# Performance work log

Hardware: AMD Instinct MI355X
Metric: run time of the kernel (lower is better)

The kernel has to match this reference:

```python
import jax, jax.numpy as jnp
import numpy as np

D = 512
B = 64
T = 512

def setup_inputs() -> dict:
    key = jax.random.key(0)
    ks = jax.random.split(key, 9)
    s = 1.0 / np.sqrt(D)
    def w(k):
        return jax.random.uniform(k, (D, D), jnp.float32, -s, s)
    def b(k):
        return jax.random.uniform(k, (D,), jnp.float32, -s, s)
    return {
        "evidence_seq": jax.random.normal(ks[0], (B, T, D), jnp.float32),
        "We": w(ks[1]), "be": b(ks[2]),
        "Wp": w(ks[3]), "bp": b(ks[4]),
        "Wl": w(ks[5]), "bl": b(ks[6]),
        "Ww": w(ks[7]), "bw": b(ks[8]),
    }

def reference(evidence_seq, We, be, Wp, bp, Wl, bl, Ww, bw):
    # Precompute all input-side projections in batched GEMMs: (B,T,D)
    ev_proj = jnp.einsum('btd,de->bte', evidence_seq, We) + be
    leak = jax.nn.sigmoid(jnp.einsum('btd,de->bte', evidence_seq, Wl) + bl)
    write = jax.nn.sigmoid(jnp.einsum('btd,de->bte', evidence_seq, Ww) + bw)

    def step(belief_prev, inputs):
        ev_t, leak_t, write_t = inputs  # each (B, D)
        candidate = jnp.tanh(belief_prev @ Wp + bp + ev_t)
        belief = leak_t * belief_prev + write_t * candidate
        return belief, belief

    belief0 = jnp.zeros((evidence_seq.shape[0], We.shape[1]), evidence_seq.dtype)
    # scan over time axis: move T to leading dim
    xs = (jnp.swapaxes(ev_proj, 0, 1), jnp.swapaxes(leak, 0, 1), jnp.swapaxes(write, 0, 1))
    _, belief_seq_t = jax.lax.scan(step, belief0, xs)
    return jnp.swapaxes(belief_seq_t, 0, 1)  # (B, T, D)
```

## Files before the change

### kernel.cpp

```cpp
#include <hip/hip_runtime.h>
#include <math.h>

#define DD 512
#define TT 512

typedef __attribute__((ext_vector_type(8))) short short8;
typedef __attribute__((ext_vector_type(4))) float float4v;

static __device__ inline unsigned short f2bf(float f) {
    unsigned int b = __builtin_bit_cast(unsigned int, f);
    b += 0x7FFFu + ((b >> 16) & 1u);
    return (unsigned short)(b >> 16);
}
static __device__ inline float bf2f(unsigned short u) {
    unsigned int b = ((unsigned int)u) << 16;
    return __builtin_bit_cast(float, b);
}

__global__ __launch_bounds__(512) void proj_kernel(
    const float* __restrict__ X,
    const float* __restrict__ We, const float* __restrict__ be,
    const float* __restrict__ Wl, const float* __restrict__ bl,
    const float* __restrict__ Ww, const float* __restrict__ bw,
    float* __restrict__ Pe, unsigned short* __restrict__ Pl,
    unsigned short* __restrict__ Pw)
{
    __shared__ __align__(16) unsigned short Asw[8][64][8];
    __shared__ __align__(16) unsigned short Bsw[32][64][8];

    const int tid  = threadIdx.x;
    const int lane = tid & 63;
    const int wv   = tid >> 6;
    const int mat  = blockIdx.y;
    const int m0   = blockIdx.x * 128;

    const float* W    = (mat == 0) ? We : (mat == 1 ? Wl : Ww);
    const float* bias = (mat == 0) ? be : (mat == 1 ? bl : bw);

    float4v acc[32];
#pragma unroll
    for (int i = 0; i < 32; i++) acc[i] = (float4v){0.f, 0.f, 0.f, 0.f};

    for (int kc = 0; kc < 16; kc++) {
        __syncthreads();
#pragma unroll
        for (int i = 0; i < 2; i++) {
            int f = tid + 512 * i;
            int m = f >> 3;
            int k = (f & 7) * 4;
            float4v xv = *reinterpret_cast<const float4v*>(
                &X[(m0 + m) * DD + kc * 32 + k]);
            int mt = m >> 4;
            int ln = (m & 15) | (((k >> 3) & 3) << 4);
            int j  = k & 7;
            Asw[mt][ln][j + 0] = f2bf(xv.x);
            Asw[mt][ln][j + 1] = f2bf(xv.y);
            Asw[mt][ln][j + 2] = f2bf(xv.z);
            Asw[mt][ln][j + 3] = f2bf(xv.w);
        }
#pragma unroll
        for (int i = 0; i < 8; i++) {
            int f = tid + 512 * i;
            int k = f >> 7;
            int n = (f & 127) * 4;
            float4v wv4 = *reinterpret_cast<const float4v*>(
                &W[(kc * 32 + k) * DD + n]);
            int q  = (k >> 3) & 3;
            int j  = k & 7;
            int nt = n >> 4;
            int lb = (n & 15) | (q << 4);
            Bsw[nt][lb + 0][j] = f2bf(wv4.x);
            Bsw[nt][lb + 1][j] = f2bf(wv4.y);
            Bsw[nt][lb + 2][j] = f2bf(wv4.z);
            Bsw[nt][lb + 3][j] = f2bf(wv4.w);
        }
        __syncthreads();
        short8 a = *reinterpret_cast<const short8*>(&Asw[wv][lane][0]);
#pragma unroll
        for (int nt = 0; nt < 32; nt++) {
            short8 b = *reinterpret_cast<const short8*>(&Bsw[nt][lane][0]);
            acc[nt] = __builtin_amdgcn_mfma_f32_16x16x32_bf16(a, b, acc[nt], 0, 0, 0);
        }
    }

    const int q  = lane >> 4;
    const int c0 = lane & 15;
#pragma unroll
    for (int nt = 0; nt < 32; nt++) {
        int   col = nt * 16 + c0;
        float bv  = bias[col];
#pragma unroll
        for (int r = 0; r < 4; r++) {
            int row = m0 + wv * 16 + q * 4 + r;
            float v = acc[nt][r] + bv;
            int idx = row * DD + col;
            if (mat == 0) {
                Pe[idx] = v;
            } else {
                float s = 1.0f / (1.0f + expf(-v));
                if (mat == 1) Pl[idx] = f2bf(s);
                else          Pw[idx] = f2bf(s);
            }
        }
    }
}

__global__ __launch_bounds__(512) void rec_kernel(
    const float* __restrict__ Wp, const float* __restrict__ bp,
    const float* __restrict__ Pe, const unsigned short* __restrict__ Pl,
    const unsigned short* __restrict__ Pw,
    float* __restrict__ dout, unsigned* ex)
{
    __shared__ __align__(16) unsigned short Bsw[8][16][64][8];
    __shared__ __align__(16) unsigned short Asw[16][520];

    const int tid  = threadIdx.x;
    const int lane = tid & 63;
    const int wv   = tid >> 6;
    const int team = blockIdx.x & 7;
    const int wsl  = blockIdx.x >> 3;
    const int m0   = team * 8;
    const int n0   = wsl * 128;

    for (int i = 0; i < 32; i++) {
        int f  = tid + 512 * i;
        int k  = f >> 5;
        int nl = (f & 31) * 4;
        float4v w4 = *reinterpret_cast<const float4v*>(&Wp[k * DD + n0 + nl]);
        int kk = k >> 5;
        int qq = (k >> 3) & 3;
        int j  = k & 7;
        int nt = nl >> 4;
        int lb = (nl & 15) | (qq << 4);
        Bsw[nt][kk][lb + 0][j] = f2bf(w4.x);
        Bsw[nt][kk][lb + 1][j] = f2bf(w4.y);
        Bsw[nt][kk][lb + 2][j] = f2bf(w4.z);
        Bsw[nt][kk][lb + 3][j] = f2bf(w4.w);
    }
    for (int i = tid; i < 16 * 520; i += 512) ((unsigned short*)Asw)[i] = 0;
    __syncthreads();

    const int  qf     = lane >> 4;
    const int  c0     = lane & 15;
    const bool active = (qf < 2);
    const int  nep    = n0 + wv * 16 + c0;
    const int  ts     = wv * 32 + qf * 16 + c0;
    const float bpv   = bp[nep];
    float pv[4] = {0.f, 0.f, 0.f, 0.f};

    int pp[3];
#pragma unroll
    for (int p3 = 0; p3 < 3; p3++) pp[p3] = p3 + (p3 >= wsl ? 1 : 0);

    for (int t = 0; t < TT; t++) {
        float pe[4], lk[4], wr[4];
        int   idx[4];
        if (active) {
#pragma unroll
            for (int r = 0; r < 4; r++) {
                int brow = m0 + qf * 4 + r;
                idx[r] = (brow * TT + t) * DD + nep;
                pe[r]  = Pe[idx[r]];
                lk[r]  = bf2f(Pl[idx[r]]);
                wr[r]  = bf2f(Pw[idx[r]]);
            }
        }

        if (t > 0 && active) {
            const unsigned tg = (unsigned)(t - 1);
            unsigned* exb = ex + (unsigned)(((t - 1) & 1) * 8 + team) * 4096;
            const unsigned* ap[3];
#pragma unroll
            for (int p3 = 0; p3 < 3; p3++)
                ap[p3] = exb + pp[p3] * 1024 + ts * 4;

            unsigned w[12];
            bool ok;
            do {
#pragma unroll
                for (int p3 = 0; p3 < 3; p3++)
#pragma unroll
                    for (int r = 0; r < 4; r++)
                        w[p3 * 4 + r] = __hip_atomic_load(
                            ap[p3] + r, __ATOMIC_RELAXED, __HIP_MEMORY_SCOPE_AGENT);
                ok = true;
#pragma unroll
                for (int i = 0; i < 12; i++) ok &= ((w[i] & 0xFFFFu) == tg);
            } while (!ok);

#pragma unroll
            for (int p3 = 0; p3 < 3; p3++) {
                int col = pp[p3] * 128 + wv * 16 + c0;
#pragma unroll
                for (int r = 0; r < 4; r++)
                    Asw[qf * 4 + r][col] = (unsigned short)(w[p3 * 4 + r] >> 16);
            }
        }
        __syncthreads();

        float4v acc0 = {0.f, 0.f, 0.f, 0.f}, acc1 = {0.f, 0.f, 0.f, 0.f};
#pragma unroll
        for (int kk = 0; kk < 16; kk++) {
            short8 a = *reinterpret_cast<const short8*>(&Asw[c0][kk * 32 + qf * 8]);
            short8 b = *reinterpret_cast<const short8*>(&Bsw[wv][kk][lane][0]);
            if (kk & 1) acc1 = __builtin_amdgcn_mfma_f32_16x16x32_bf16(a, b, acc1, 0, 0, 0);
            else        acc0 = __builtin_amdgcn_mfma_f32_16x16x32_bf16(a, b, acc0, 0, 0, 0);
        }

        float bel[4];
        if (active) {
#pragma unroll
            for (int r = 0; r < 4; r++) {
                float pre  = acc0[r] + acc1[r] + bpv + pe[r];
                float cand = tanhf(pre);
                bel[r] = lk[r] * pv[r] + wr[r] * cand;
                pv[r]  = bel[r];
            }
        }
        __syncthreads();

        if (active) {
#pragma unroll
            for (int r = 0; r < 4; r++) Asw[qf * 4 + r][nep] = f2bf(bel[r]);
            unsigned* sp = ex + (unsigned)((t & 1) * 8 + team) * 4096
                              + wsl * 1024 + ts * 4;
#pragma unroll
            for (int r = 0; r < 4; r++) {
                unsigned wd = ((unsigned)f2bf(bel[r]) << 16) | (unsigned)(t & 0xFFFF);
                __hip_atomic_store(sp + r, wd, __ATOMIC_RELAXED,
                                   __HIP_MEMORY_SCOPE_AGENT);
            }
#pragma unroll
            for (int r = 0; r < 4; r++) dout[idx[r]] = bel[r];
        }
    }
}

extern "C" void kernel_launch(void* const* d_in, const int* in_sizes, int n_in,
                              void* d_out, int out_size, void* d_ws, size_t ws_size,
                              hipStream_t stream) {
    (void)in_sizes; (void)n_in; (void)out_size; (void)ws_size;
    const float* X  = (const float*)d_in[0];
    const float* We = (const float*)d_in[1];
    const float* be = (const float*)d_in[2];
    const float* Wp = (const float*)d_in[3];
    const float* bp = (const float*)d_in[4];
    const float* Wl = (const float*)d_in[5];
    const float* bl = (const float*)d_in[6];
    const float* Ww = (const float*)d_in[7];
    const float* bw = (const float*)d_in[8];
    float* out = (float*)d_out;

    char* ws = (char*)d_ws;
    float*          Pe = (float*)ws;
    unsigned short* Pl = (unsigned short*)(ws + 67108864);
    unsigned short* Pw = (unsigned short*)(ws + 100663296);
    unsigned*       ex = (unsigned*)(ws + 134217728);

    proj_kernel<<<dim3(256, 3), 512, 0, stream>>>(X, We, be, Wl, bl, Ww, bw,
                                                  Pe, Pl, Pw);
    rec_kernel<<<dim3(32), 512, 0, stream>>>(Wp, bp, Pe, Pl, Pw, out, ex);
}
```

Baseline: 2.023 ms.

## Replace cross-block atomic exchange with independent per-batch-slice recurrence blocks

The recurrence was split across 32 blocks that swapped belief slices every step through global atomics and spin-waits. It now runs on 4 blocks, each owning 16 batch rows and the full 512-wide Wp, so the per-step exchange uses only shared memory and __syncthreads. Most of Wp is held in registers as bf16, the belief tile in LDS is XOR-swizzled, and tanh is computed with __expf. The projection kernel now folds bp into the Pe bias, stores Pe as bf16 instead of fp32, and writes all three projections in a per-timestep page layout so each step reads contiguous uint2 loads. The trade-off is much less parallelism (4 CUs) with 4x more MFMA work per block, plus reduced precision on Pe.

After: 3.600 ms. 1.78x slower.

```diff
diff --git a/kernel.cpp b/kernel.cpp
--- a/kernel.cpp
+++ b/kernel.cpp
@@ -12,18 +12,21 @@
     b += 0x7FFFu + ((b >> 16) & 1u);
     return (unsigned short)(b >> 16);
 }
-static __device__ inline float bf2f(unsigned short u) {
-    unsigned int b = ((unsigned int)u) << 16;
-    return __builtin_bit_cast(float, b);
+static __device__ inline float bfhi(unsigned u) {
+    return __builtin_bit_cast(float, u & 0xFFFF0000u);
+}
+static __device__ inline float bflo(unsigned u) {
+    return __builtin_bit_cast(float, u << 16);
 }
 
 __global__ __launch_bounds__(512) void proj_kernel(
     const float* __restrict__ X,
     const float* __restrict__ We, const float* __restrict__ be,
+    const float* __restrict__ bp,
     const float* __restrict__ Wl, const float* __restrict__ bl,
     const float* __restrict__ Ww, const float* __restrict__ bw,
-    float* __restrict__ Pe, unsigned short* __restrict__ Pl,
-    unsigned short* __restrict__ Pw)
+    unsigned short* __restrict__ PeB, unsigned short* __restrict__ Pl2,
+    unsigned short* __restrict__ Pw2)
 {
     __shared__ __align__(16) unsigned short Asw[8][64][8];
     __shared__ __align__(16) unsigned short Bsw[32][64][8];
@@ -34,8 +37,7 @@
     const int mat  = blockIdx.y;
     const int m0   = blockIdx.x * 128;
 
-    const float* W    = (mat == 0) ? We : (mat == 1 ? Wl : Ww);
-    const float* bias = (mat == 0) ? be : (mat == 1 ? bl : bw);
+    const float* W = (mat == 0) ? We : (mat == 1 ? Wl : Ww);
 
     float4v acc[32];
 #pragma unroll
@@ -83,156 +85,152 @@
         }
     }
 
-    const int q  = lane >> 4;
-    const int c0 = lane & 15;
-#pragma unroll
-    for (int nt = 0; nt < 32; nt++) {
-        int   col = nt * 16 + c0;
-        float bv  = bias[col];
+    const int q     = lane >> 4;
+    const int c0    = lane & 15;
+    const int tbase = m0 & 511;
+    const int rb    = m0 >> 9;
+    const int b     = rb >> 4;
+    const int qft   = (rb & 15) >> 2;
+    const int rt    = rb & 3;
+
+    unsigned short* P = (mat == 0) ? PeB : (mat == 1 ? Pl2 : Pw2);
+
+#pragma unroll
+    for (int wt = 0; wt < 8; wt++) {
+        const int tidt = wt * 64 + qft * 16 + c0;
+        float bs[4];
+#pragma unroll
+        for (int n2 = 0; n2 < 4; n2++) {
+            const int col = (wt * 4 + n2) * 16 + c0;
+            bs[n2] = (mat == 0) ? (be[col] + bp[col])
+                                : ((mat == 1) ? bl[col] : bw[col]);
+        }
 #pragma unroll
         for (int r = 0; r < 4; r++) {
-            int row = m0 + wv * 16 + q * 4 + r;
-            float v = acc[nt][r] + bv;
-            int idx = row * DD + col;
-            if (mat == 0) {
-                Pe[idx] = v;
-            } else {
-                float s = 1.0f / (1.0f + expf(-v));
-                if (mat == 1) Pl[idx] = f2bf(s);
-                else          Pw[idx] = f2bf(s);
+            const int t    = tbase + wv * 16 + q * 4 + r;
+            const int page = (((t << 2) + b) << 2) + rt;
+            float v[4];
+#pragma unroll
+            for (int n2 = 0; n2 < 4; n2++) {
+                float x = acc[wt * 4 + n2][r] + bs[n2];
+                v[n2] = (mat == 0) ? x : (1.0f / (1.0f + expf(-x)));
             }
+            uint2 u;
+            u.x = (unsigned)f2bf(v[0]) | ((unsigned)f2bf(v[1]) << 16);
+            u.y = (unsigned)f2bf(v[2]) | ((unsigned)f2bf(v[3]) << 16);
+            *reinterpret_cast<uint2*>(&P[(page << 11) + (tidt << 2)]) = u;
         }
     }
 }
 
 __global__ __launch_bounds__(512) void rec_kernel(
-    const float* __restrict__ Wp, const float* __restrict__ bp,
-    const float* __restrict__ Pe, const unsigned short* __restrict__ Pl,
-    const unsigned short* __restrict__ Pw,
-    float* __restrict__ dout, unsigned* ex)
+    const float* __restrict__ Wp,
+    const unsigned short* __restrict__ PeB,
+    const unsigned short* __restrict__ Pl2,
+    const unsigned short* __restrict__ Pw2,
+    float* __restrict__ dout)
 {
-    __shared__ __align__(16) unsigned short Bsw[8][16][64][8];
-    __shared__ __align__(16) unsigned short Asw[16][520];
+    __shared__ __align__(16) unsigned short BswL[8][16][64][8];
+    __shared__ __align__(16) char AswP[16384];
 
     const int tid  = threadIdx.x;
     const int lane = tid & 63;
     const int wv   = tid >> 6;
-    const int team = blockIdx.x & 7;
-    const int wsl  = blockIdx.x >> 3;
-    const int m0   = team * 8;
-    const int n0   = wsl * 128;
-
-    for (int i = 0; i < 32; i++) {
-        int f  = tid + 512 * i;
-        int k  = f >> 5;
-        int nl = (f & 31) * 4;
-        float4v w4 = *reinterpret_cast<const float4v*>(&Wp[k * DD + n0 + nl]);
-        int kk = k >> 5;
-        int qq = (k >> 3) & 3;
-        int j  = k & 7;
-        int nt = nl >> 4;
-        int lb = (nl & 15) | (qq << 4);
-        Bsw[nt][kk][lb + 0][j] = f2bf(w4.x);
-        Bsw[nt][kk][lb + 1][j] = f2bf(w4.y);
-        Bsw[nt][kk][lb + 2][j] = f2bf(w4.z);
-        Bsw[nt][kk][lb + 3][j] = f2bf(w4.w);
-    }
-    for (int i = tid; i < 16 * 520; i += 512) ((unsigned short*)Asw)[i] = 0;
+    const int qf   = lane >> 4;
+    const int c0   = lane & 15;
+    const int blk  = blockIdx.x;
+
+    short8 bf[3][16];
+
+#pragma unroll
+    for (int nt = 0; nt < 4; nt++) {
+        for (int it = 0; it < 32; it++) {
+            const int f  = it * 64 + lane;
+            const int k  = f >> 2;
+            const int c4 = f & 3;
+            const float4v w4 = *reinterpret_cast<const float4v*>(
+                &Wp[(k << 9) + wv * 64 + nt * 16 + c4 * 4]);
+            const int kk = k >> 5;
+            const int qq = (k >> 3) & 3;
+            const int j  = k & 7;
+            const int lb = (c4 * 4) | (qq << 4);
+            BswL[wv][kk][lb + 0][j] = f2bf(w4.x);
+            BswL[wv][kk][lb + 1][j] = f2bf(w4.y);
+            BswL[wv][kk][lb + 2][j] = f2bf(w4.z);
+            BswL[wv][kk][lb + 3][j] = f2bf(w4.w);
+        }
+        if (nt < 3) {
+#pragma unroll
+            for (int kk = 0; kk < 16; kk++)
+                bf[nt][kk] = *reinterpret_cast<const short8*>(&BswL[wv][kk][lane][0]);
+        }
+    }
+
+#pragma unroll
+    for (int i = 0; i < 8; i++)
+        reinterpret_cast<unsigned*>(AswP)[tid + (i << 9)] = 0;
     __syncthreads();
 
-    const int  qf     = lane >> 4;
-    const int  c0     = lane & 15;
-    const bool active = (qf < 2);
-    const int  nep    = n0 + wv * 16 + c0;
-    const int  ts     = wv * 32 + qf * 16 + c0;
-    const float bpv   = bp[nep];
-    float pv[4] = {0.f, 0.f, 0.f, 0.f};
-
-    int pp[3];
-#pragma unroll
-    for (int p3 = 0; p3 < 3; p3++) pp[p3] = p3 + (p3 >= wsl ? 1 : 0);
+    float pv[4][4];
+#pragma unroll
+    for (int nt = 0; nt < 4; nt++)
+#pragma unroll
+        for (int r = 0; r < 4; r++) pv[nt][r] = 0.0f;
+
+    const int colb = wv * 64 + c0;
+    const int aswz = (c0 & 7) << 4;
+    const int arp  = (c0 << 10) + (qf << 4);
+    const int bq   = (blk << 4) + (qf << 2);
 
     for (int t = 0; t < TT; t++) {
-        float pe[4], lk[4], wr[4];
-        int   idx[4];
-        if (active) {
+        float4v acc[4];
+#pragma unroll
+        for (int i = 0; i < 4; i++) acc[i] = (float4v){0.f, 0.f, 0.f, 0.f};
+#pragma unroll
+        for (int kk = 0; kk < 16; kk++) {
+            const short8 a = *reinterpret_cast<const short8*>(
+                AswP + ((arp + (kk << 6)) ^ aswz));
+            const short8 b3 = *reinterpret_cast<const short8*>(&BswL[wv][kk][lane][0]);
+            acc[0] = __builtin_amdgcn_mfma_f32_16x16x32_bf16(a, bf[0][kk], acc[0], 0, 0, 0);
+            acc[1] = __builtin_amdgcn_mfma_f32_16x16x32_bf16(a, bf[1][kk], acc[1], 0, 0, 0);
+            acc[2] = __builtin_amdgcn_mfma_f32_16x16x32_bf16(a, bf[2][kk], acc[2], 0, 0, 0);
+            acc[3] = __builtin_amdgcn_mfma_f32_16x16x32_bf16(a, b3,        acc[3], 0, 0, 0);
+        }
+        __syncthreads();
+
+        const int pgb = ((t << 2) + blk) << 2;
+        uint2 pe2[4], lk2[4], wr2[4];
+#pragma unroll
+        for (int r = 0; r < 4; r++) {
+            const int off = ((pgb + r) << 11) + (tid << 2);
+            pe2[r] = *reinterpret_cast<const uint2*>(&PeB[off]);
+            lk2[r] = *reinterpret_cast<const uint2*>(&Pl2[off]);
+            wr2[r] = *reinterpret_cast<const uint2*>(&Pw2[off]);
+        }
+
+#pragma unroll
+        for (int nt = 0; nt < 4; nt++) {
 #pragma unroll
             for (int r = 0; r < 4; r++) {
-                int brow = m0 + qf * 4 + r;
-                idx[r] = (brow * TT + t) * DD + nep;
-                pe[r]  = Pe[idx[r]];
-                lk[r]  = bf2f(Pl[idx[r]]);
-                wr[r]  = bf2f(Pw[idx[r]]);
+                const unsigned pu = (nt < 2) ? pe2[r].x : pe2[r].y;
+                const unsigned lu = (nt < 2) ? lk2[r].x : lk2[r].y;
+                const unsigned wu = (nt < 2) ? wr2[r].x : wr2[r].y;
+                const float pef = (nt & 1) ? bfhi(pu) : bflo(pu);
+                const float lkf = (nt & 1) ? bfhi(lu) : bflo(lu);
+                const float wrf = (nt & 1) ? bfhi(wu) : bflo(wu);
+                const float pre  = acc[nt][r] + pef;
+                const float e    = __expf(2.0f * pre);
+                const float cand = 1.0f - 2.0f / (e + 1.0f);
+                const float bel  = lkf * pv[nt][r] + wrf * cand;
+                pv[nt][r] = bel;
+                dout[((bq + r) << 18) + (t << 9) + colb + nt * 16] = bel;
+                const int rl = (qf << 2) + r;
+                const int wb = (((rl << 10) + ((colb + nt * 16) << 1))
+                                ^ ((rl & 7) << 4));
+                *reinterpret_cast<unsigned short*>(AswP + wb) = f2bf(bel);
             }
         }
-
-        if (t > 0 && active) {
-            const unsigned tg = (unsigned)(t - 1);
-            unsigned* exb = ex + (unsigned)(((t - 1) & 1) * 8 + team) * 4096;
-            const unsigned* ap[3];
-#pragma unroll
-            for (int p3 = 0; p3 < 3; p3++)
-                ap[p3] = exb + pp[p3] * 1024 + ts * 4;
-
-            unsigned w[12];
-            bool ok;
-            do {
-#pragma unroll
-                for (int p3 = 0; p3 < 3; p3++)
-#pragma unroll
-                    for (int r = 0; r < 4; r++)
-                        w[p3 * 4 + r] = __hip_atomic_load(
-                            ap[p3] + r, __ATOMIC_RELAXED, __HIP_MEMORY_SCOPE_AGENT);
-                ok = true;
-#pragma unroll
-                for (int i = 0; i < 12; i++) ok &= ((w[i] & 0xFFFFu) == tg);
-            } while (!ok);
-
-#pragma unroll
-            for (int p3 = 0; p3 < 3; p3++) {
-                int col = pp[p3] * 128 + wv * 16 + c0;
-#pragma unroll
-                for (int r = 0; r < 4; r++)
-                    Asw[qf * 4 + r][col] = (unsigned short)(w[p3 * 4 + r] >> 16);
-            }
-        }
-        __syncthreads();
-
-        float4v acc0 = {0.f, 0.f, 0.f, 0.f}, acc1 = {0.f, 0.f, 0.f, 0.f};
-#pragma unroll
-        for (int kk = 0; kk < 16; kk++) {
-            short8 a = *reinterpret_cast<const short8*>(&Asw[c0][kk * 32 + qf * 8]);
-            short8 b = *reinterpret_cast<const short8*>(&Bsw[wv][kk][lane][0]);
-            if (kk & 1) acc1 = __builtin_amdgcn_mfma_f32_16x16x32_bf16(a, b, acc1, 0, 0, 0);
-            else        acc0 = __builtin_amdgcn_mfma_f32_16x16x32_bf16(a, b, acc0, 0, 0, 0);
-        }
-
-        float bel[4];
-        if (active) {
-#pragma unroll
-            for (int r = 0; r < 4; r++) {
-                float pre  = acc0[r] + acc1[r] + bpv + pe[r];
-                float cand = tanhf(pre);
-                bel[r] = lk[r] * pv[r] + wr[r] * cand;
-                pv[r]  = bel[r];
-            }
-        }
-        __syncthreads();
-
-        if (active) {
-#pragma unroll
-            for (int r = 0; r < 4; r++) Asw[qf * 4 + r][nep] = f2bf(bel[r]);
-            unsigned* sp = ex + (unsigned)((t & 1) * 8 + team) * 4096
-                              + wsl * 1024 + ts * 4;
-#pragma unroll
-            for (int r = 0; r < 4; r++) {
-                unsigned wd = ((unsigned)f2bf(bel[r]) << 16) | (unsigned)(t & 0xFFFF);
-                __hip_atomic_store(sp + r, wd, __ATOMIC_RELAXED,
-                                   __HIP_MEMORY_SCOPE_AGENT);
-            }
-#pragma unroll
-            for (int r = 0; r < 4; r++) dout[idx[r]] = bel[r];
-        }
+        __syncthreads();
     }
 }
 
@@ -252,12 +250,11 @@
     float* out = (float*)d_out;
 
     char* ws = (char*)d_ws;
-    float*          Pe = (float*)ws;
-    unsigned short* Pl = (unsigned short*)(ws + 67108864);
-    unsigned short* Pw = (unsigned short*)(ws + 100663296);
-    unsigned*       ex = (unsigned*)(ws + 134217728);
-
-    proj_kernel<<<dim3(256, 3), 512, 0, stream>>>(X, We, be, Wl, bl, Ww, bw,
-                                                  Pe, Pl, Pw);
-    rec_kernel<<<dim3(32), 512, 0, stream>>>(Wp, bp, Pe, Pl, Pw, out, ex);
-}
+    unsigned short* PeB = (unsigned short*)ws;
+    unsigned short* Pl2 = (unsigned short*)(ws + 33554432);
+    unsigned short* Pw2 = (unsigned short*)(ws + 67108864);
+
+    proj_kernel<<<dim3(256, 3), 512, 0, stream>>>(X, We, be, bp, Wl, bl,
+                                                  Ww, bw, PeB, Pl2, Pw2);
+    rec_kernel<<<dim3(4), 512, 0, stream>>>(Wp, PeB, Pl2, Pw2, out);
+}
```
